# Performance work log

Measured on AMD Instinct MI355X. Metric: run time of the kernel, lower is better.

The kernel has to match this reference:

```python
import jax, jax.numpy as jnp
import numpy as np

B, C, H, W = 8, 256, 64, 64
HEADS = 8
DH = C // HEADS          # dim_head = in_ch // heads (as constructed in BasicTransBlock)
RS = 16                  # reduce_size
EPS = 1e-5               # BatchNorm eps


def _rel_pos_index():
    # Swin-style relative position index over the RS x RS reduced grid
    coords = np.stack(np.meshgrid(np.arange(RS), np.arange(RS), indexing='ij')).reshape(2, -1)
    rel = coords[:, :, None] - coords[:, None, :]
    rel = rel.transpose(1, 2, 0).copy()
    rel[:, :, 0] += RS - 1
    rel[:, :, 1] += RS - 1
    rel[:, :, 0] *= 2 * RS - 1
    return jnp.asarray(rel.sum(-1))  # [RS*RS, RS*RS] int

REL_IDX = _rel_pos_index()


def setup_inputs() -> dict:
    key = jax.random.key(0)
    ks = jax.random.split(key, 8)
    f32 = jnp.float32
    return {
        "x": jax.random.normal(ks[0], (B, C, H, W), f32),
        "bn1_gamma": jnp.ones((C,), f32),
        "bn1_beta": jnp.zeros((C,), f32),
        "bn1_mean": jnp.zeros((C,), f32),
        "bn1_var": jnp.ones((C,), f32),
        "qkv_dw": jax.random.normal(ks[1], (C, 1, 3, 3), f32) * 0.05,   # depthwise 3x3
        "qkv_pw": jax.random.normal(ks[2], (3 * C, C), f32) * 0.05,     # pointwise 1x1 -> 3C
        "out_dw": jax.random.normal(ks[3], (C, 1, 3, 3), f32) * 0.05,
        "out_pw": jax.random.normal(ks[4], (C, C), f32) * 0.05,
        "rel_table": jax.random.normal(ks[5], ((2 * RS - 1) ** 2, HEADS), f32) * 0.02,
        "bn2_gamma": jnp.ones((C,), f32),
        "bn2_beta": jnp.zeros((C,), f32),
        "bn2_mean": jnp.zeros((C,), f32),
        "bn2_var": jnp.ones((C,), f32),
        "mlp_w": jax.random.normal(ks[6], (C, C), f32) * 0.05,          # 1x1 conv, no bias
    }


def _bn(x, gamma, beta, mean, var):
    # inference-mode BatchNorm2d
    inv = gamma * jax.lax.rsqrt(var + EPS)
    return x * inv[None, :, None, None] + (beta - mean * inv)[None, :, None, None]


def _dwconv3(x, w):
    # depthwise 3x3, stride 1, padding 1
    return jax.lax.conv_general_dilated(
        x, w, (1, 1), 'SAME', feature_group_count=x.shape[1],
        dimension_numbers=('NCHW', 'OIHW', 'NCHW'))


def _interp_ac(x, oh, ow):
    # bilinear resize, align_corners=True (matches F.interpolate(..., align_corners=True))
    _, _, h, w = x.shape
    ys = jnp.linspace(0.0, h - 1.0, oh)
    xs = jnp.linspace(0.0, w - 1.0, ow)
    y0 = jnp.floor(ys).astype(jnp.int32); y1 = jnp.minimum(y0 + 1, h - 1)
    x0 = jnp.floor(xs).astype(jnp.int32); x1 = jnp.minimum(x0 + 1, w - 1)
    wy = (ys - y0.astype(ys.dtype))[:, None]   # [oh,1]
    wx = (xs - x0.astype(xs.dtype))            # [ow]
    v = x[:, :, y0, :] * (1 - wy) + x[:, :, y1, :] * wy      # [B,C,oh,w]
    return v[:, :, :, x0] * (1 - wx) + v[:, :, :, x1] * wx   # [B,C,oh,ow]


def _split_heads(t, h, w):
    # channel layout in rearrange is (dim_head heads): c = d*HEADS + head
    b = t.shape[0]
    return t.reshape(b, DH, HEADS, h * w).transpose(0, 2, 3, 1)  # [B,heads,hw,DH]


def _rel_bias(rel_table):
    bias = rel_table[REL_IDX.reshape(-1)].reshape(RS, RS, RS * RS, HEADS)
    bias = jnp.repeat(bias, H // RS, axis=0)   # expand rows to H
    bias = jnp.repeat(bias, W // RS, axis=1)   # expand cols to W
    return bias.reshape(H * W, RS * RS, HEADS).transpose(2, 0, 1)  # [heads, HW, RS*RS]


def reference(x, bn1_gamma, bn1_beta, bn1_mean, bn1_var,
              qkv_dw, qkv_pw, out_dw, out_pw, rel_table,
              bn2_gamma, bn2_beta, bn2_mean, bn2_var, mlp_w):
    out = _bn(x, bn1_gamma, bn1_beta, bn1_mean, bn1_var)

    # --- LinearAttention ---
    qkv = jnp.einsum('bchw,oc->bohw', _dwconv3(out, qkv_dw), qkv_pw)
    q, k, v = jnp.split(qkv, 3, axis=1)
    k = _interp_ac(k, RS, RS)
    v = _interp_ac(v, RS, RS)
    q = _split_heads(q, H, W)       # [B,heads,HW,DH]
    k = _split_heads(k, RS, RS)     # [B,heads,RS^2,DH]
    v = _split_heads(v, RS, RS)
    attn = jnp.einsum('bhid,bhjd->bhij', q, k)
    attn = (attn + _rel_bias(rel_table)[None]) * (DH ** -0.5)  # bias added BEFORE scale, as in source
    attn = jax.nn.softmax(attn, axis=-1)
    o = jnp.einsum('bhij,bhjd->bhid', attn, v)                 # [B,heads,HW,DH]
    o = o.transpose(0, 3, 1, 2).reshape(x.shape[0], C, H, W)   # inverse of (dim_head heads) split
    o = jnp.einsum('bchw,oc->bohw', _dwconv3(o, out_dw), out_pw)

    out = o + x
    residue = out
    out = jax.nn.relu(_bn(out, bn2_gamma, bn2_beta, bn2_mean, bn2_var))
    out = jnp.einsum('bchw,oc->bohw', out, mlp_w)
    return out + residue
```

## Files before the change

### kernel.cpp

```cpp
#include <hip/hip_runtime.h>
#include <hip/hip_bf16.h>
#include <math.h>

#define EPSF 1e-5f

typedef float f32x4 __attribute__((ext_vector_type(4)));
typedef short short8 __attribute__((ext_vector_type(8)));
typedef short short4v __attribute__((ext_vector_type(4)));
typedef unsigned short u16x4 __attribute__((ext_vector_type(4)));
typedef unsigned short u16x8 __attribute__((ext_vector_type(8)));

static __device__ __forceinline__ unsigned short f2bf(float f) {
    unsigned u = __float_as_uint(f);
    u = (u + 0x7FFF + ((u >> 16) & 1)) >> 16;
    return (unsigned short)u;
}

static __device__ __forceinline__ float bf2f(unsigned short u) {
    return __uint_as_float((unsigned)u << 16);
}

static __device__ __forceinline__ unsigned packbf2(float a, float b) {
    __hip_bfloat162 t = __float22bfloat162_rn(float2{a, b});
    union { __hip_bfloat162 v; unsigned u; } cv;
    cv.v = t;
    return cv.u;
}

static __device__ __forceinline__ int swz(int r) { return ((r ^ (r >> 2)) & 7) << 1; }

#define ATTN_SCALE 0.17677669529663687f

template<bool BN, bool IB, bool OBF>
__global__ __launch_bounds__(256) void dwconv_k(
    const void* __restrict__ X, const float* __restrict__ DW,
    const float* __restrict__ g, const float* __restrict__ be,
    const float* __restrict__ mn, const float* __restrict__ vr,
    void* __restrict__ Out)
{
    int tid = threadIdx.x;
    int plane = blockIdx.x * 2 + (tid >> 7);
    int c = plane & 255;
    float inv = 1.f, ad = 0.f;
    if (BN) {
        inv = g[c] * rsqrtf(vr[c] + EPSF);
        ad  = be[c] - mn[c] * inv;
    }
    float w[9];
#pragma unroll
    for (int i = 0; i < 9; ++i) w[i] = DW[c * 9 + i];
    const float* Xf          = (const float*)X + (size_t)plane * 4096;
    const unsigned short* Xh = (const unsigned short*)X + (size_t)plane * 4096;
    int u  = tid & 127;
    int y0 = (u >> 3) * 4;
    int x0 = (u & 7) * 8;

    float r[6][16];
#pragma unroll
    for (int rr = 0; rr < 6; ++rr) {
        int yy = y0 + rr - 1;
        bool rv = (unsigned)yy < 64u;
#pragma unroll
        for (int gq = 0; gq < 4; ++gq) {
            int xx = x0 - 4 + gq * 4;
            f32x4 v = {0.f, 0.f, 0.f, 0.f};
            if (rv && (unsigned)xx < 64u) {
                if (IB) {
                    u16x4 u4 = *(const u16x4*)&Xh[yy * 64 + xx];
                    v[0] = bf2f(u4[0]); v[1] = bf2f(u4[1]);
                    v[2] = bf2f(u4[2]); v[3] = bf2f(u4[3]);
                } else {
                    v = *(const f32x4*)&Xf[yy * 64 + xx];
                }
                if (BN) {
#pragma unroll
                    for (int j = 0; j < 4; ++j) v[j] = v[j] * inv + ad;
                }
            }
            r[rr][gq * 4 + 0] = v[0]; r[rr][gq * 4 + 1] = v[1];
            r[rr][gq * 4 + 2] = v[2]; r[rr][gq * 4 + 3] = v[3];
        }
    }

#pragma unroll
    for (int j = 0; j < 4; ++j) {
        float acc[8] = {};
#pragma unroll
        for (int ky = 0; ky < 3; ++ky) {
#pragma unroll
            for (int kx = 0; kx < 3; ++kx) {
                float ww = w[ky * 3 + kx];
#pragma unroll
                for (int p = 0; p < 8; ++p)
                    acc[p] += ww * r[j + ky][3 + p + kx];
            }
        }
        if (OBF) {
            unsigned short* Ob = (unsigned short*)Out + (size_t)plane * 4096;
            int4 pk = { (int)packbf2(acc[0], acc[1]), (int)packbf2(acc[2], acc[3]),
                        (int)packbf2(acc[4], acc[5]), (int)packbf2(acc[6], acc[7]) };
            *(int4*)&Ob[(y0 + j) * 64 + x0] = pk;
        } else {
            float* Ob = (float*)Out + (size_t)plane * 4096;
            f32x4 lo = {acc[0], acc[1], acc[2], acc[3]};
            f32x4 hi = {acc[4], acc[5], acc[6], acc[7]};
            *(f32x4*)&Ob[(y0 + j) * 64 + x0]     = lo;
            *(f32x4*)&Ob[(y0 + j) * 64 + x0 + 4] = hi;
        }
    }
}

__global__ __launch_bounds__(256) void interp_k(
    const unsigned short* __restrict__ T, float* __restrict__ R)
{
    int bc = blockIdx.x;
    const unsigned short* Tb = T + (size_t)bc * 4096;
    int p  = threadIdx.x;
    int oy = p >> 4, ox = p & 15;
    const float st = 63.0f / 15.0f;
    float fy = oy * st, fx = ox * st;
    int y0 = (int)floorf(fy); int y1 = min(y0 + 1, 63); float wy = fy - (float)y0;
    int x0 = (int)floorf(fx); int x1 = min(x0 + 1, 63); float wx = fx - (float)x0;
    float v00 = bf2f(Tb[y0 * 64 + x0]), v01 = bf2f(Tb[y0 * 64 + x1]);
    float v10 = bf2f(Tb[y1 * 64 + x0]), v11 = bf2f(Tb[y1 * 64 + x1]);
    R[(size_t)bc * 256 + p] =
        (1.f - wy) * ((1.f - wx) * v00 + wx * v01) +
        wy         * ((1.f - wx) * v10 + wx * v11);
}

__global__ __launch_bounds__(256) void bias_k(
    const float* __restrict__ rel, float* __restrict__ btab)
{
    int idx = blockIdx.x * 256 + threadIdx.x;
    int h   = idx >> 16;
    int qc  = (idx >> 8) & 255;
    int key = idx & 255;
    int ay = qc >> 4, ax = qc & 15, by = key >> 4, bx = key & 15;
    int t = (ay - by + 15) * 31 + (ax - bx + 15);
    btab[idx] = rel[t * 8 + h] * ATTN_SCALE;
}

__global__ __launch_bounds__(256) void kvt_k(
    const unsigned short* __restrict__ kv,
    unsigned short* __restrict__ khat, unsigned short* __restrict__ vhat)
{
    __shared__ unsigned short kt_[32 * 260];
    int bh = blockIdx.x;
    int b = bh >> 3, h = bh & 7;
    const unsigned short* kvb = kv + (size_t)b * 512 * 256;
    int tid = threadIdx.x;

#pragma unroll
    for (int it = 0; it < 8; ++it) {
        int idx = it * 256 + tid;
        int d = idx >> 6, k4 = (idx & 63) * 4;
        ushort4 v = *(const ushort4*)&kvb[(size_t)(256 + d * 8 + h) * 256 + k4];
        *(ushort4*)&vhat[(size_t)bh * 8192 + d * 256 + k4] = v;
    }
#pragma unroll
    for (int it = 0; it < 8; ++it) {
        int idx = it * 256 + tid;
        int d = idx >> 6, k4 = (idx & 63) * 4;
        ushort4 v = *(const ushort4*)&kvb[(size_t)(d * 8 + h) * 256 + k4];
        *(ushort4*)&kt_[d * 260 + k4] = v;
    }
    __syncthreads();
#pragma unroll
    for (int it = 0; it < 8; ++it) {
        int idx = it * 256 + tid;
        int key = idx >> 3, dq = idx & 7;
        ushort4 o;
        o.x = kt_[(dq * 4 + 0) * 260 + key];
        o.y = kt_[(dq * 4 + 1) * 260 + key];
        o.z = kt_[(dq * 4 + 2) * 260 + key];
        o.w = kt_[(dq * 4 + 3) * 260 + key];
        *(ushort4*)&khat[(size_t)bh * 8192 + key * 32 + dq * 4] = o;
    }
}

template<int MODE, bool OB, bool AB, bool QHAT>
__global__ __launch_bounds__(256) void mgemm_k(
    const void* __restrict__ A, const float* __restrict__ W,
    float* __restrict__ Out, const float* __restrict__ X,
    const float* __restrict__ g, const float* __restrict__ be,
    const float* __restrict__ mn, const float* __restrict__ vr,
    int M, int Ntot)
{
    __shared__ short Ws[128 * 256];
    __shared__ short As[128 * 64];
    int b = blockIdx.z, m0 = blockIdx.x * 128, n0 = blockIdx.y * 128;
    int tid = threadIdx.x;
    const float* Abf          = (const float*)A + (size_t)b * 256 * M;
    const unsigned short* Abh = (const unsigned short*)A + (size_t)b * 256 * M;

#pragma unroll
    for (int it = 0; it < 32; ++it) {
        int idx = it * 256 + tid;
        int n = idx >> 6, kq = idx & 63;
        f32x4 w4 = *(const f32x4*)&W[(size_t)(n0 + n) * 256 + kq * 4];
        short4v pk = { (short)f2bf(w4[0]), (short)f2bf(w4[1]),
                       (short)f2bf(w4[2]), (short)f2bf(w4[3]) };
        *(short4v*)&Ws[n * 256 + ((kq ^ swz(n)) << 2)] = pk;
    }

    int mg = tid & 31, kg = tid >> 5;
    f32x4 rg[8];
    u16x4 rg16[8];
    auto load_tile = [&](int k0) {
#pragma unroll
        for (int half = 0; half < 2; ++half) {
#pragma unroll
            for (int i = 0; i < 4; ++i) {
                int c = k0 + kg * 4 + half * 32 + i;
                if (AB) {
                    rg16[half * 4 + i] = *(const u16x4*)&Abh[(size_t)c * M + m0 + mg * 4];
                } else {
                    f32x4 v = *(const f32x4*)&Abf[(size_t)c * M + m0 + mg * 4];
                    if (MODE == 2) {
                        float iv = g[c] * rsqrtf(vr[c] + EPSF);
                        float ad = be[c] - mn[c] * iv;
#pragma unroll
                        for (int j = 0; j < 4; ++j) v[j] = fmaxf(v[j] * iv + ad, 0.f);
                    }
                    rg[half * 4 + i] = v;
                }
            }
        }
    };
    load_tile(0);

    int w = tid >> 6, lane = tid & 63;
    int wm = w & 1, wn = w >> 1;
    int lg = lane >> 4, lc = lane & 15;
    f32x4 acc[4][4] = {};

    for (int k0 = 0; k0 < 256; k0 += 64) {
        __syncthreads();
#pragma unroll
        for (int half = 0; half < 2; ++half) {
#pragma unroll
            for (int j = 0; j < 4; ++j) {
                int m = mg * 4 + j;
                short4v pk;
                if (AB) {
                    pk = short4v{ (short)rg16[half * 4 + 0][j], (short)rg16[half * 4 + 1][j],
                                  (short)rg16[half * 4 + 2][j], (short)rg16[half * 4 + 3][j] };
                } else {
                    pk = short4v{ (short)f2bf(rg[half * 4 + 0][j]), (short)f2bf(rg[half * 4 + 1][j]),
                                  (short)f2bf(rg[half * 4 + 2][j]), (short)f2bf(rg[half * 4 + 3][j]) };
                }
                *(short4v*)&As[m * 64 + (((kg + half * 8) ^ swz(m)) << 2)] = pk;
            }
        }
        __syncthreads();
        if (k0 < 192) load_tile(k0 + 64);
#pragma unroll
        for (int ksl = 0; ksl < 2; ++ksl) {
            short8 wf[4], af[4];
            int gk = (k0 + ksl * 32 + lg * 8) >> 2;
            int ga = (ksl * 32 + lg * 8) >> 2;
#pragma unroll
            for (int nt = 0; nt < 4; ++nt) {
                int n = wn * 64 + nt * 16 + lc;
                wf[nt] = *(const short8*)&Ws[n * 256 + ((gk ^ swz(n)) << 2)];
            }
#pragma unroll
            for (int mt = 0; mt < 4; ++mt) {
                int m = wm * 64 + mt * 16 + lc;
                af[mt] = *(const short8*)&As[m * 64 + ((ga ^ swz(m)) << 2)];
            }
#pragma unroll
            for (int nt = 0; nt < 4; ++nt)
#pragma unroll
                for (int mt = 0; mt < 4; ++mt)
                    acc[nt][mt] = __builtin_amdgcn_mfma_f32_16x16x32_bf16(
                        wf[nt], af[mt], acc[nt][mt], 0, 0, 0);
        }
    }

    if (QHAT) {
        __syncthreads();
        unsigned short* Os = (unsigned short*)Ws;
#pragma unroll
        for (int nt = 0; nt < 4; ++nt)
#pragma unroll
            for (int mt = 0; mt < 4; ++mt)
#pragma unroll
                for (int reg = 0; reg < 4; ++reg) {
                    int nl = wn * 64 + nt * 16 + lg * 4 + reg;
                    int ml = wm * 64 + mt * 16 + lc;
                    Os[nl * 130 + ml] = f2bf(acc[nt][mt][reg] * ATTN_SCALE);
                }
        __syncthreads();
        unsigned short* Oq = (unsigned short*)Out;
        int dbase = n0 >> 3;
#pragma unroll
        for (int it = 0; it < 4; ++it) {
            int ri = it * 256 + tid;
            int hh = ri >> 7, ml = ri & 127;
            u16x8 lo, hi;
#pragma unroll
            for (int dd = 0; dd < 8; ++dd) {
                lo[dd] = Os[(dd * 8 + hh) * 130 + ml];
                hi[dd] = Os[((dd + 8) * 8 + hh) * 130 + ml];
            }
            size_t base = ((size_t)(b * 8 + hh) * 4096 + m0 + ml) * 32 + dbase;
            *(u16x8*)&Oq[base]     = lo;
            *(u16x8*)&Oq[base + 8] = hi;
        }
        return;
    }

    size_t ob = (size_t)b * Ntot * M;
#pragma unroll
    for (int nt = 0; nt < 4; ++nt) {
#pragma unroll
        for (int mt = 0; mt < 4; ++mt) {
#pragma unroll
            for (int reg = 0; reg < 4; ++reg) {
                int n = n0 + wn * 64 + nt * 16 + lg * 4 + reg;
                int m = m0 + wm * 64 + mt * 16 + lc;
                size_t addr = ob + (size_t)n * M + m;
                float v = acc[nt][mt][reg];
                if (MODE >= 1) v += X[addr];
                if (OB) ((unsigned short*)Out)[addr] = f2bf(v);
                else    Out[addr] = v;
            }
        }
    }
}

__global__ __launch_bounds__(256) void attn_mfma_k(
    const unsigned short* __restrict__ Qh, const unsigned short* __restrict__ Khat,
    const unsigned short* __restrict__ Vhat,
    const float* __restrict__ btab, unsigned short* __restrict__ O)
{
    __shared__ float Om[2][4][16][36];
    __shared__ float Lw[2][4][16];

    int b = blockIdx.z, h = blockIdx.y, chunk = blockIdx.x;
    int tid = threadIdx.x;
    int w = tid >> 6, lane = tid & 63;
    int lg = lane >> 4, lc = lane & 15;
    int kw = w * 64;

    const unsigned short* Kb = Khat + (size_t)(b * 8 + h) * 8192;
    const unsigned short* Vb = Vhat + (size_t)(b * 8 + h) * 8192;
    const unsigned short* Qb = Qh + (size_t)(b * 8 + h) * 131072;
    unsigned short* Ob = O + (size_t)b * 256 * 4096;
    const float* bt = btab + (size_t)h * 65536;
    int rw = chunk * 128;

    int s1 = ((lg & 1) << 5) + lc;
    int s2 = s1 + 16;
    bool useOdd = (lg >> 1) != 0;
    int mrow = tid & 15, md = tid >> 4;

    short8 kf[4], vf0[2], vf1[2];
#pragma unroll
    for (int kt = 0; kt < 4; ++kt)
        kf[kt] = *(const short8*)&Kb[(kw + kt * 16 + lc) * 32 + lg * 8];
#pragma unroll
    for (int ks = 0; ks < 2; ++ks) {
        vf0[ks] = *(const short8*)&Vb[lc * 256 + kw + ks * 32 + lg * 8];
        vf1[ks] = *(const short8*)&Vb[(16 + lc) * 256 + kw + ks * 32 + lg * 8];
    }

    auto compute = [&](int mt, int buf) {
        int rbase = rw + mt * 16;
        int r_a = rbase + lc;
        int qc = ((r_a >> 8) << 4) | ((r_a >> 2) & 15);
        const float* bq = bt + (size_t)qc * 256 + kw + lg * 4;

        f32x4 sacc[4];
#pragma unroll
        for (int kt = 0; kt < 4; ++kt)
            sacc[kt] = *(const f32x4*)&bq[kt * 16];

        short8 qf = *(const short8*)&Qb[(size_t)r_a * 32 + lg * 8];

#pragma unroll
        for (int kt = 0; kt < 4; ++kt)
            sacc[kt] = __builtin_amdgcn_mfma_f32_16x16x32_bf16(kf[kt], qf, sacc[kt], 0, 0, 0);

        float ls = 0.f;
        unsigned plo[4], phi[4];
#pragma unroll
        for (int kt = 0; kt < 4; ++kt) {
            float p0 = __expf(sacc[kt][0]);
            float p1 = __expf(sacc[kt][1]);
            float p2 = __expf(sacc[kt][2]);
            float p3 = __expf(sacc[kt][3]);
            ls += (p0 + p1) + (p2 + p3);
            plo[kt] = packbf2(p0, p1);
            phi[kt] = packbf2(p2, p3);
        }
        ls += __shfl_xor(ls, 16);
        ls += __shfl_xor(ls, 32);

        f32x4 o0 = {0.f, 0.f, 0.f, 0.f}, o1 = {0.f, 0.f, 0.f, 0.f};
#pragma unroll
        for (int ks = 0; ks < 2; ++ks) {
            int eA = __shfl((int)plo[2 * ks], s1), oA = __shfl((int)plo[2 * ks + 1], s1);
            int eB = __shfl((int)phi[2 * ks], s1), oB = __shfl((int)phi[2 * ks + 1], s1);
            int eC = __shfl((int)plo[2 * ks], s2), oC = __shfl((int)plo[2 * ks + 1], s2);
            int eD = __shfl((int)phi[2 * ks], s2), oD = __shfl((int)phi[2 * ks + 1], s2);
            int4 pi = { useOdd ? oA : eA, useOdd ? oB : eB,
                        useOdd ? oC : eC, useOdd ? oD : eD };
            short8 pf = *(short8*)&pi;
            o0 = __builtin_amdgcn_mfma_f32_16x16x32_bf16(vf0[ks], pf, o0, 0, 0, 0);
            o1 = __builtin_amdgcn_mfma_f32_16x16x32_bf16(vf1[ks], pf, o1, 0, 0, 0);
        }

        *(f32x4*)&Om[buf][w][lc][lg * 4]      = o0;
        *(f32x4*)&Om[buf][w][lc][16 + lg * 4] = o1;
        if (lg == 0) Lw[buf][w][lc] = ls;
    };

    auto merge = [&](int mt, int buf) {
        int rbase = rw + mt * 16;
        float L = Lw[buf][0][mrow] + Lw[buf][1][mrow]
                + Lw[buf][2][mrow] + Lw[buf][3][mrow];
        float inv = 1.f / L;
        float a0 = Om[buf][0][mrow][md] + Om[buf][1][mrow][md]
                 + Om[buf][2][mrow][md] + Om[buf][3][mrow][md];
        float a1 = Om[buf][0][mrow][md + 16] + Om[buf][1][mrow][md + 16]
                 + Om[buf][2][mrow][md + 16] + Om[buf][3][mrow][md + 16];
        Ob[(size_t)(md * 8 + h) * 4096 + rbase + mrow]        = f2bf(a0 * inv);
        Ob[(size_t)((md + 16) * 8 + h) * 4096 + rbase + mrow] = f2bf(a1 * inv);
    };

    compute(0, 0);
    for (int mt = 0; mt < 8; ++mt) {
        __syncthreads();
        if (mt < 7) compute(mt + 1, (mt + 1) & 1);
        merge(mt, mt & 1);
    }
}

extern "C" void kernel_launch(void* const* d_in, const int* in_sizes, int n_in,
                              void* d_out, int out_size, void* d_ws, size_t ws_size,
                              hipStream_t stream)
{
    const float* x       = (const float*)d_in[0];
    const float* bn1_g   = (const float*)d_in[1];
    const float* bn1_b   = (const float*)d_in[2];
    const float* bn1_m   = (const float*)d_in[3];
    const float* bn1_v   = (const float*)d_in[4];
    const float* qkv_dw  = (const float*)d_in[5];
    const float* qkv_pw  = (const float*)d_in[6];
    const float* out_dw  = (const float*)d_in[7];
    const float* out_pw  = (const float*)d_in[8];
    const float* rel     = (const float*)d_in[9];
    const float* bn2_g   = (const float*)d_in[10];
    const float* bn2_b   = (const float*)d_in[11];
    const float* bn2_m   = (const float*)d_in[12];
    const float* bn2_v   = (const float*)d_in[13];
    const float* mlp_w   = (const float*)d_in[14];
    float* out = (float*)d_out;

    float* ws = (float*)d_ws;
    float* t    = ws;
    float* q    = ws + (size_t)8 * 1024 * 1024;
    float* tr   = ws + (size_t)16 * 1024 * 1024;
    float* kv   = tr + 524288;
    float* btab = kv + 524288;
    float* khat = btab + 524288;
    float* vhat = khat + 262144;
    float* o   = t;
    float* t2  = q;
    float* a   = t;

    bias_k<<<dim3(2048), 256, 0, stream>>>(rel, btab);

    dwconv_k<true, false, true><<<dim3(1024), 256, 0, stream>>>(
        x, qkv_dw, bn1_g, bn1_b, bn1_m, bn1_v, t);

    mgemm_k<0, true, true, true><<<dim3(32, 2, 8), 256, 0, stream>>>(
        t, qkv_pw, q, nullptr, nullptr, nullptr, nullptr, nullptr,
        4096, 256);

    interp_k<<<dim3(2048), 256, 0, stream>>>((const unsigned short*)t, tr);

    mgemm_k<0, true, false, false><<<dim3(2, 4, 8), 256, 0, stream>>>(
        tr, qkv_pw + 256 * 256, kv, nullptr, nullptr, nullptr, nullptr, nullptr,
        256, 512);

    kvt_k<<<dim3(64), 256, 0, stream>>>(
        (const unsigned short*)kv, (unsigned short*)khat, (unsigned short*)vhat);

    attn_mfma_k<<<dim3(32, 8, 8), 256, 0, stream>>>(
        (const unsigned short*)q, (const unsigned short*)khat,
        (const unsigned short*)vhat, btab, (unsigned short*)o);

    dwconv_k<false, true, true><<<dim3(1024), 256, 0, stream>>>(
        o, out_dw, nullptr, nullptr, nullptr, nullptr, t2);

    mgemm_k<1, false, true, false><<<dim3(32, 2, 8), 256, 0, stream>>>(
        t2, out_pw, a, x, nullptr, nullptr, nullptr, nullptr,
        4096, 256);

    mgemm_k<2, false, false, false><<<dim3(32, 2, 8), 256, 0, stream>>>(
        a, mlp_w, out, a, bn2_g, bn2_b, bn2_m, bn2_v,
        4096, 256);
}
```

Baseline: 134.8 us.

## Fuse output projection, residual, BN2+ReLU and MLP GEMM into one kernel

```diff
diff --git a/kernel.cpp b/kernel.cpp
--- a/kernel.cpp
+++ b/kernel.cpp
@@ -325,6 +325,154 @@
                 if (MODE >= 1) v += X[addr];
                 if (OB) ((unsigned short*)Out)[addr] = f2bf(v);
                 else    Out[addr] = v;
+            }
+        }
+    }
+}
+
+__global__ __launch_bounds__(256) void ffn_k(
+    const unsigned short* __restrict__ T2, const float* __restrict__ Wo,
+    const float* __restrict__ Wm, const float* __restrict__ X,
+    const float* __restrict__ g, const float* __restrict__ be,
+    const float* __restrict__ mn, const float* __restrict__ vr,
+    float* __restrict__ Out)
+{
+    __shared__ short Ws[256 * 64];
+    __shared__ short As[64 * 64];
+    __shared__ short As2[64 * 256];
+
+    int b = blockIdx.z;
+    int m0 = blockIdx.x * 64;
+    int tid = threadIdx.x;
+    int w = tid >> 6, lane = tid & 63;
+    int lg = lane >> 4, lc = lane & 15;
+    const unsigned short* Ab = T2 + (size_t)b * 256 * 4096;
+    int mg = tid & 15, kg = tid >> 4;
+
+    f32x4 acc1[4][4] = {};
+
+    for (int k0 = 0; k0 < 256; k0 += 64) {
+        __syncthreads();
+        u16x4 rg16[4];
+#pragma unroll
+        for (int i = 0; i < 4; ++i)
+            rg16[i] = *(const u16x4*)&Ab[(size_t)(k0 + kg * 4 + i) * 4096 + m0 + mg * 4];
+#pragma unroll
+        for (int j = 0; j < 4; ++j) {
+            int m = mg * 4 + j;
+            short4v pk = { (short)rg16[0][j], (short)rg16[1][j],
+                           (short)rg16[2][j], (short)rg16[3][j] };
+            *(short4v*)&As[m * 64 + ((kg ^ swz(m)) << 2)] = pk;
+        }
+        {
+            int n = tid;
+#pragma unroll
+            for (int kq = 0; kq < 16; ++kq) {
+                f32x4 w4 = *(const f32x4*)&Wo[(size_t)n * 256 + k0 + kq * 4];
+                short4v pk = { (short)f2bf(w4[0]), (short)f2bf(w4[1]),
+                               (short)f2bf(w4[2]), (short)f2bf(w4[3]) };
+                *(short4v*)&Ws[n * 64 + ((kq ^ swz(n)) << 2)] = pk;
+            }
+        }
+        __syncthreads();
+#pragma unroll
+        for (int ksl = 0; ksl < 2; ++ksl) {
+            int gk = ksl * 8 + lg * 2;
+            short8 wf[4], af[4];
+#pragma unroll
+            for (int nt = 0; nt < 4; ++nt) {
+                int n = w * 64 + nt * 16 + lc;
+                wf[nt] = *(const short8*)&Ws[n * 64 + ((gk ^ swz(n)) << 2)];
+            }
+#pragma unroll
+            for (int mt = 0; mt < 4; ++mt) {
+                int m = mt * 16 + lc;
+                af[mt] = *(const short8*)&As[m * 64 + ((gk ^ swz(m)) << 2)];
+            }
+#pragma unroll
+            for (int nt = 0; nt < 4; ++nt)
+#pragma unroll
+                for (int mt = 0; mt < 4; ++mt)
+                    acc1[nt][mt] = __builtin_amdgcn_mfma_f32_16x16x32_bf16(
+                        wf[nt], af[mt], acc1[nt][mt], 0, 0, 0);
+        }
+    }
+
+    const float* Xb = X + (size_t)b * 256 * 4096;
+#pragma unroll
+    for (int nt = 0; nt < 4; ++nt) {
+        int cbase = w * 64 + nt * 16 + lg * 4;
+        float iv[4], ad[4];
+#pragma unroll
+        for (int reg = 0; reg < 4; ++reg) {
+            int c = cbase + reg;
+            iv[reg] = g[c] * rsqrtf(vr[c] + EPSF);
+            ad[reg] = be[c] - mn[c] * iv[reg];
+        }
+#pragma unroll
+        for (int mt = 0; mt < 4; ++mt) {
+            int m = m0 + mt * 16 + lc;
+#pragma unroll
+            for (int reg = 0; reg < 4; ++reg)
+                acc1[nt][mt][reg] += Xb[(size_t)(cbase + reg) * 4096 + m];
+            int ml = mt * 16 + lc;
+            short4v pk = {
+                (short)f2bf(fmaxf(acc1[nt][mt][0] * iv[0] + ad[0], 0.f)),
+                (short)f2bf(fmaxf(acc1[nt][mt][1] * iv[1] + ad[1], 0.f)),
+                (short)f2bf(fmaxf(acc1[nt][mt][2] * iv[2] + ad[2], 0.f)),
+                (short)f2bf(fmaxf(acc1[nt][mt][3] * iv[3] + ad[3], 0.f)) };
+            *(short4v*)&As2[ml * 256 + (((cbase >> 2) ^ swz(ml)) << 2)] = pk;
+        }
+    }
+
+    f32x4 acc2[4][4] = {};
+    for (int k0 = 0; k0 < 256; k0 += 64) {
+        __syncthreads();
+        {
+            int n = tid;
+#pragma unroll
+            for (int kq = 0; kq < 16; ++kq) {
+                f32x4 w4 = *(const f32x4*)&Wm[(size_t)n * 256 + k0 + kq * 4];
+                short4v pk = { (short)f2bf(w4[0]), (short)f2bf(w4[1]),
+                               (short)f2bf(w4[2]), (short)f2bf(w4[3]) };
+                *(short4v*)&Ws[n * 64 + ((kq ^ swz(n)) << 2)] = pk;
+            }
+        }
+        __syncthreads();
+#pragma unroll
+        for (int ksl = 0; ksl < 2; ++ksl) {
+            int gkw = ksl * 8 + lg * 2;
+            int gka = (k0 >> 2) + ksl * 8 + lg * 2;
+            short8 wf[4], af[4];
+#pragma unroll
+            for (int nt = 0; nt < 4; ++nt) {
+                int n = w * 64 + nt * 16 + lc;
+                wf[nt] = *(const short8*)&Ws[n * 64 + ((gkw ^ swz(n)) << 2)];
+            }
+#pragma unroll
+            for (int mt = 0; mt < 4; ++mt) {
+                int m = mt * 16 + lc;
+                af[mt] = *(const short8*)&As2[m * 256 + ((gka ^ swz(m)) << 2)];
+            }
+#pragma unroll
+            for (int nt = 0; nt < 4; ++nt)
+#pragma unroll
+                for (int mt = 0; mt < 4; ++mt)
+                    acc2[nt][mt] = __builtin_amdgcn_mfma_f32_16x16x32_bf16(
+                        wf[nt], af[mt], acc2[nt][mt], 0, 0, 0);
+        }
+    }
+
+    float* Ob = Out + (size_t)b * 256 * 4096;
+#pragma unroll
+    for (int nt = 0; nt < 4; ++nt) {
+#pragma unroll
+        for (int mt = 0; mt < 4; ++mt) {
+#pragma unroll
+            for (int reg = 0; reg < 4; ++reg) {
+                int n = w * 64 + nt * 16 + lg * 4 + reg;
+                int m = m0 + mt * 16 + lc;
+                Ob[(size_t)n * 4096 + m] = acc2[nt][mt][reg] + acc1[nt][mt][reg];
             }
         }
     }
@@ -469,7 +617,6 @@
     float* vhat = khat + 262144;
     float* o   = t;
     float* t2  = q;
-    float* a   = t;
 
     bias_k<<<dim3(2048), 256, 0, stream>>>(rel, btab);
 
@@ -496,11 +643,7 @@
     dwconv_k<false, true, true><<<dim3(1024), 256, 0, stream>>>(
         o, out_dw, nullptr, nullptr, nullptr, nullptr, t2);
 
-    mgemm_k<1, false, true, false><<<dim3(32, 2, 8), 256, 0, stream>>>(
-        t2, out_pw, a, x, nullptr, nullptr, nullptr, nullptr,
-        4096, 256);
-
-    mgemm_k<2, false, false, false><<<dim3(32, 2, 8), 256, 0, stream>>>(
-        a, mlp_w, out, a, bn2_g, bn2_b, bn2_m, bn2_v,
-        4096, 256);
-}
+    ffn_k<<<dim3(64, 1, 8), 256, 0, stream>>>(
+        (const unsigned short*)t2, out_pw, mlp_w, x,
+        bn2_g, bn2_b, bn2_m, bn2_v, out);
+}
```

Measured after the change: 138.0 us. 2.4% more time.
